# Performance work log

Measured on AMD Instinct MI355X. Metric: run time of the kernel, lower is better.

The kernel has to match this reference:

```python
import jax, jax.numpy as jnp
import numpy as np

B, S, D = 2, 2048, 2048
H, HD = 16, 128
ROPE_THETA = 10000.0


def _rope_cos_sin(seq_len, head_dim, dtype=jnp.float32):
    inv_freq = 1.0 / (ROPE_THETA ** (jnp.arange(0, head_dim, 2, dtype=jnp.float32) / head_dim))
    t = jnp.arange(seq_len, dtype=jnp.float32)
    freqs = jnp.outer(t, inv_freq)                     # [S, HD/2]
    emb = jnp.concatenate([freqs, freqs], axis=-1)     # [S, HD]
    return jnp.cos(emb).astype(dtype), jnp.sin(emb).astype(dtype)


def _rotate_half(x):
    x1, x2 = jnp.split(x, 2, axis=-1)
    return jnp.concatenate([-x2, x1], axis=-1)


def _apply_rope(x, cos, sin):
    # x: [B, S, H, HD]; cos/sin: [S, HD] -> broadcast over batch and heads
    c = cos[None, :, None, :]
    s = sin[None, :, None, :]
    return x * c + _rotate_half(x) * s


def setup_inputs() -> dict:
    key = jax.random.key(0)
    ks = jax.random.split(key, 6)
    scale = 1.0 / np.sqrt(D)
    hidden_states = jax.random.normal(ks[0], (B, S, D), dtype=jnp.float32)
    # causal additive mask: 0 on/below diagonal, large negative above
    neg = jnp.finfo(jnp.float32).min
    causal = jnp.where(jnp.tril(jnp.ones((S, S), dtype=bool)), 0.0, neg)
    attention_mask = jnp.broadcast_to(causal[None, None, :, :], (B, 1, S, S)).astype(jnp.float32)
    Wq = jax.random.normal(ks[1], (D, D), dtype=jnp.float32) * scale
    Wk = jax.random.normal(ks[2], (D, D), dtype=jnp.float32) * scale
    Wv = jax.random.normal(ks[3], (D, D), dtype=jnp.float32) * scale
    Wo = jax.random.normal(ks[4], (D, D), dtype=jnp.float32) * scale
    return {"hidden_states": hidden_states, "attention_mask": attention_mask,
            "Wq": Wq, "Wk": Wk, "Wv": Wv, "Wo": Wo}


def reference(hidden_states, attention_mask, Wq, Wk, Wv, Wo):
    b, s, d = hidden_states.shape
    # projections (torch Linear: x @ W^T)
    q = (hidden_states @ Wq.T).reshape(b, s, H, HD)
    k = (hidden_states @ Wk.T).reshape(b, s, H, HD)
    v = (hidden_states @ Wv.T).reshape(b, s, H, HD)
    cos, sin = _rope_cos_sin(s, HD, hidden_states.dtype)
    q = _apply_rope(q, cos, sin)
    k = _apply_rope(k, cos, sin)
    # naive attention, [B, H, S, S] scores materialized as in the original
    scores = jnp.einsum('bqhd,bkhd->bhqk', q, k) / np.sqrt(HD)
    scores = scores + attention_mask
    attn = jax.nn.softmax(scores, axis=-1)
    out = jnp.einsum('bhqk,bkhd->bqhd', attn, v).reshape(b, s, d)
    return out @ Wo.T
```

## Files before the change

kernel.cpp:

```cpp
#include <hip/hip_runtime.h>
#include <hip/hip_bf16.h>

typedef __hip_bfloat16 bf16;
typedef __attribute__((ext_vector_type(8))) short s16x8;
typedef __attribute__((ext_vector_type(4))) float f32x4;
typedef __attribute__((ext_vector_type(16))) float f32x16;

#define MFMA16(a, b, c) __builtin_amdgcn_mfma_f32_16x16x32_bf16(a, b, c, 0, 0, 0)
#define MFMA32(a, b, c) __builtin_amdgcn_mfma_f32_32x32x16_bf16(a, b, c, 0, 0, 0)

#define GLL16(gsrc, ldst)                                                                 \
  __builtin_amdgcn_global_load_lds(                                                       \
      (const __attribute__((address_space(1))) unsigned int*)(gsrc),                      \
      (__attribute__((address_space(3))) unsigned int*)(ldst), 16, 0, 0)

#define VMCNT(n) asm volatile("s_waitcnt vmcnt(" #n ")" ::: "memory")
#define BARRIER() __builtin_amdgcn_s_barrier()

static constexpr int S_LEN = 2048;
static constexpr int D_DIM = 2048;
static constexpr int NY = 6144;

union BF4 { ushort4 u; bf16 b[4]; };

__device__ inline unsigned pack2(float a, float b) {
  union { bf16 h[2]; unsigned u; } x;
  x.h[0] = __float2bfloat16(a);
  x.h[1] = __float2bfloat16(b);
  return x.u;
}

__global__ void convert_all(const float* __restrict__ X, const float* __restrict__ Wq,
                            const float* __restrict__ Wk, const float* __restrict__ Wv,
                            const float* __restrict__ Wo, bf16* __restrict__ Xb,
                            bf16* __restrict__ Wb, bf16* __restrict__ Wob,
                            float* __restrict__ cosT, float* __restrict__ sinT) {
  int gid = blockIdx.x * 256 + threadIdx.x;
  if (gid < 6291456) {
    int i4 = gid * 4;
    const float* src;
    bf16* dst;
    int off;
    if (i4 < 8388608) {
      src = X; dst = Xb; off = i4;
    } else {
      int j = i4 - 8388608;
      int seg = j >> 22;
      off = j & 4194303;
      if (seg == 0) { src = Wq; dst = Wb; }
      else if (seg == 1) { src = Wk; dst = Wb + 4194304; }
      else if (seg == 2) { src = Wv; dst = Wb + 8388608; }
      else { src = Wo; dst = Wob; }
    }
    float4 v = *(const float4*)(src + off);
    BF4 o;
    o.b[0] = __float2bfloat16(v.x);
    o.b[1] = __float2bfloat16(v.y);
    o.b[2] = __float2bfloat16(v.z);
    o.b[3] = __float2bfloat16(v.w);
    *(ushort4*)(dst + off) = o.u;
  } else {
    int t4 = (gid - 6291456) * 4;
    if (t4 < 131072) {
#pragma unroll
      for (int k = 0; k < 4; ++k) {
        int i = t4 + k;
        int d = i & 63, s = i >> 6;
        float inv = powf(10000.0f, -(float)d * (1.0f / 64.0f));
        float ang = (float)s * inv;
        cosT[i] = cosf(ang);
        sinT[i] = sinf(ang);
      }
    }
  }
}

__global__ __launch_bounds__(256) void rope_tv(bf16* __restrict__ Y,
                                               const float* __restrict__ cosT,
                                               const float* __restrict__ sinT,
                                               bf16* __restrict__ Vt) {
  __shared__ bf16 tile[32][36];
  const int bid = blockIdx.x;
  const int t = threadIdx.x;
  if (bid < 8192) {
    int idx = bid * 256 + t;
    int quad = idx & 15;
    int h = (idx >> 4) & 15;
    int m = (idx >> 8) & 4095;
    int g = idx >> 20;
    int s = m & (S_LEN - 1);
    int d0 = quad * 4;
    float sc = g ? 1.0f : 0.08838834764831845f * 1.4426950408889634f;
    bf16* p = Y + (size_t)m * NY + g * D_DIM + h * 128 + d0;
    BF4 lo, hi, olo, ohi;
    lo.u = *(const ushort4*)p;
    hi.u = *(const ushort4*)(p + 64);
    float4 c = *(const float4*)(cosT + s * 64 + d0);
    float4 sn = *(const float4*)(sinT + s * 64 + d0);
    float cc[4] = {c.x, c.y, c.z, c.w};
    float ss[4] = {sn.x, sn.y, sn.z, sn.w};
#pragma unroll
    for (int i = 0; i < 4; ++i) {
      float x1 = __bfloat162float(lo.b[i]);
      float x2 = __bfloat162float(hi.b[i]);
      olo.b[i] = __float2bfloat16((x1 * cc[i] - x2 * ss[i]) * sc);
      ohi.b[i] = __float2bfloat16((x2 * cc[i] + x1 * ss[i]) * sc);
    }
    *(ushort4*)p = olo.u;
    *(ushort4*)(p + 64) = ohi.u;
  } else {
    int id = bid - 8192;
    int bx = id & 63, by = (id >> 6) & 3, bh = id >> 8;
    int b = bh >> 4, h = bh & 15;
    int s0 = bx * 32, d0 = by * 32;
    int r = t >> 3;
    int c4 = (t & 7) * 4;
    BF4 in;
    in.u = *(const ushort4*)(Y + (size_t)(b * S_LEN + s0 + r) * NY + 4096 + h * 128 + d0 + c4);
    *(ushort4*)(&tile[r][c4]) = in.u;
    __syncthreads();
    BF4 o;
#pragma unroll
    for (int i = 0; i < 4; ++i) o.b[i] = tile[c4 + i][r];
    *(ushort4*)(Vt + (size_t)bh * 128 * S_LEN + (size_t)(d0 + r) * S_LEN + s0 + c4) = o.u;
  }
}

__device__ inline void storeC(float* p, float v) { *p = v; }
__device__ inline void storeC(bf16* p, float v) { *p = __float2bfloat16(v); }

__global__ __launch_bounds__(512, 2) void gemm256(const bf16* __restrict__ A,
                                                  const bf16* __restrict__ Bm,
                                                  bf16* __restrict__ C, int K, int lda,
                                                  int ldb, int ldc, int mt) {
  __shared__ __align__(16) char lds[131072];
  char* A0buf = lds;
  char* B0buf = lds + 32768;
  char* A1buf = lds + 65536;
  char* B1buf = lds + 98304;
  const int tid = threadIdx.x;
  const int lane = tid & 63;
  const int w = tid >> 6;
  const int wm = w >> 2, wn = w & 3;
  const int l15 = lane & 15, lh4 = lane >> 4;
  const int xr = l15 & 7;
  const int xo0 = ((lh4 ^ xr) << 4);
  const int xo1 = (((4 + lh4) ^ xr) << 4);

  const int nwg = gridDim.x;
  const int bid = blockIdx.x;
  const int swz = (bid & 7) * (nwg >> 3) + (bid >> 3);
  const int bm = swz % mt, bn = swz / mt;
  const int row0 = bm * 256, col0 = bn * 256;

  const int srow8 = lane >> 3;
  const int scol = ((lane & 7) ^ srow8) * 8;
  const bf16* gA_s = A + (size_t)(row0 + w * 8 + srow8) * lda + scol;
  const bf16* gB_s = Bm + (size_t)(col0 + (w >> 2) * 64 + (w & 3) * 8 + srow8) * ldb + scol;
  const int ldst = w * 1024;

#define STAGE_A(bufa, rh, k0)                                                     \
  {                                                                               \
    GLL16(gA_s + (size_t)((rh)*64) * lda + (k0), (bufa) + (rh)*16384 + ldst);     \
    GLL16(gA_s + (size_t)((rh)*64 + 128) * lda + (k0),                            \
          (bufa) + (rh)*16384 + 8192 + ldst);                                     \
  }
#define STAGE_B(bufb, ch, k0)                                                     \
  {                                                                               \
    GLL16(gB_s + (size_t)((ch)*32) * ldb + (k0), (bufb) + (ch)*16384 + ldst);     \
    GLL16(gB_s + (size_t)((ch)*32 + 128) * ldb + (k0),                            \
          (bufb) + (ch)*16384 + 8192 + ldst);                                     \
  }

  f32x4 acc[8][4];
#pragma unroll
  for (int i = 0; i < 8; ++i)
#pragma unroll
    for (int j = 0; j < 4; ++j) acc[i][j] = (f32x4){0.f, 0.f, 0.f, 0.f};

  s16x8 af[4][2];
  s16x8 bfr[2][2];

#define READ_AH(bufa, rh)                                                         \
  _Pragma("unroll") for (int ii = 0; ii < 4; ++ii) {                              \
    const char* p_ = (bufa) + (rh)*16384 + (wm * 64 + ii * 16 + l15) * 128;       \
    af[ii][0] = *(const s16x8*)(p_ + xo0);                                        \
    af[ii][1] = *(const s16x8*)(p_ + xo1);                                        \
  }
#define READ_BH(bufb, ch)                                                         \
  _Pragma("unroll") for (int jj = 0; jj < 2; ++jj) {                              \
    const char* p_ = (bufb) + (ch)*16384 + (wn * 32 + jj * 16 + l15) * 128;       \
    bfr[jj][0] = *(const s16x8*)(p_ + xo0);                                       \
    bfr[jj][1] = *(const s16x8*)(p_ + xo1);                                       \
  }
#define QUAD(rh, ch)                                                              \
  __builtin_amdgcn_s_setprio(1);                                                  \
  _Pragma("unroll") for (int jj = 0; jj < 2; ++jj)                                \
  _Pragma("unroll") for (int ii = 0; ii < 4; ++ii)                                \
  _Pragma("unroll") for (int ks = 0; ks < 2; ++ks)                                \
      acc[(rh)*4 + ii][(ch)*2 + jj] =                                             \
          MFMA16(af[ii][ks], bfr[jj][ks], acc[(rh)*4 + ii][(ch)*2 + jj]);         \
  __builtin_amdgcn_s_setprio(0);

  STAGE_A(A0buf, 0, 0);
  STAGE_B(B0buf, 0, 0);
  STAGE_B(B0buf, 1, 0);
  STAGE_A(A0buf, 1, 0);
  STAGE_A(A1buf, 0, 64);
  STAGE_B(B1buf, 1, 64);
  STAGE_A(A1buf, 1, 64);
  VMCNT(6);
  BARRIER();

  const int NI = K >> 7;
  for (int i = 0; i < NI; ++i) {
    const int kT1 = (2 * i + 1) << 6;
    const int kT2 = (2 * i + 2) << 6;
    const int kT3 = (2 * i + 3) << 6;
    const bool nl = (i + 1 < NI);
    READ_AH(A0buf, 0);
    READ_BH(B0buf, 0);
    STAGE_B(B1buf, 0, kT1);
    BARRIER();
    QUAD(0, 0);
    BARRIER();
    READ_BH(B0buf, 1);
    if (nl) STAGE_A(A0buf, 0, kT2);
    BARRIER();
    QUAD(0, 1);
    BARRIER();
    READ_AH(A0buf, 1);
    if (nl) STAGE_B(B0buf, 1, kT2);
    BARRIER();
    QUAD(1, 1);
    BARRIER();
    READ_BH(B0buf, 0);
    if (nl) STAGE_A(A0buf, 1, kT2);
    BARRIER();
    QUAD(1, 0);
    if (nl) { VMCNT(6); } else { VMCNT(0); }
    BARRIER();
    READ_AH(A1buf, 0);
    READ_BH(B1buf, 0);
    if (nl) STAGE_B(B0buf, 0, kT2);
    BARRIER();
    QUAD(0, 0);
    BARRIER();
    READ_BH(B1buf, 1);
    if (nl) STAGE_A(A1buf, 0, kT3);
    BARRIER();
    QUAD(0, 1);
    BARRIER();
    READ_AH(A1buf, 1);
    if (nl) STAGE_B(B1buf, 1, kT3);
    BARRIER();
    QUAD(1, 1);
    BARRIER();
    READ_BH(B1buf, 0);
    if (nl) STAGE_A(A1buf, 1, kT3);
    BARRIER();
    QUAD(1, 0);
    if (nl) { VMCNT(6); }
    BARRIER();
  }
#undef STAGE_A
#undef STAGE_B
#undef READ_AH
#undef READ_BH
#undef QUAD

#pragma unroll
  for (int ri = 0; ri < 8; ++ri)
#pragma unroll
    for (int cj = 0; cj < 4; ++cj) {
      int gr = row0 + wm * 128 + ri * 16 + lh4 * 4;
      int gc = col0 + wn * 64 + cj * 16 + l15;
#pragma unroll
      for (int rr = 0; rr < 4; ++rr)
        C[(size_t)(gr + rr) * ldc + gc] = __float2bfloat16(acc[ri][cj][rr]);
    }
}

template <typename OutT>
__global__ __launch_bounds__(512, 2) void gemm_fine(const bf16* __restrict__ A,
                                                    const bf16* __restrict__ Bm,
                                                    OutT* __restrict__ C, int K, int lda,
                                                    int ldb, int ldc, int mt) {
  __shared__ __align__(16) char lds[147456];
  char* b0 = lds;
  char* b1 = lds + 49152;
  char* b2 = lds + 98304;
  const int tid = threadIdx.x;
  const int lane = tid & 63;
  const int w = tid >> 6;
  const int wm = w >> 2, wn = w & 3;
  const int l15 = lane & 15, lh4 = lane >> 4;
  const int xr = l15 & 7;
  const int xo0 = ((lh4 ^ xr) << 4);
  const int xo1 = (((4 + lh4) ^ xr) << 4);

  const int nwg = gridDim.x;
  const int bid = blockIdx.x;
  const int swz = (bid & 7) * (nwg >> 3) + (bid >> 3);
  const int bm = swz % mt, bn = swz / mt;
  const int row0 = bm * 128, col0 = bn * 256;

  const int srow = w * 8 + (lane >> 3);
  const int scol = ((lane & 7) ^ (lane >> 3)) * 8;
  const bf16* gA = A + (size_t)(row0 + srow) * lda + scol;
  const bf16* gB = Bm + (size_t)(col0 + srow) * ldb + scol;
  const int ldst = w * 1024;

  f32x4 acc[4][4];
#pragma unroll
  for (int i = 0; i < 4; ++i)
#pragma unroll
    for (int j = 0; j < 4; ++j) acc[i][j] = (f32x4){0.f, 0.f, 0.f, 0.f};

  s16x8 af[4], bfr[4];

#define PH_READ(BUF, XO)                                                          \
  _Pragma("unroll") for (int ii = 0; ii < 4; ++ii)                                \
      af[ii] = *(const s16x8*)((BUF) + (wm * 64 + ii * 16 + l15) * 128 + (XO));   \
  _Pragma("unroll") for (int jj = 0; jj < 4; ++jj)                                \
      bfr[jj] = *(const s16x8*)((BUF) + 16384 + (wn * 64 + jj * 16 + l15) * 128 + (XO));
#define PH_FMA()                                                                  \
  __builtin_amdgcn_s_setprio(1);                                                  \
  _Pragma("unroll") for (int jj = 0; jj < 4; ++jj)                                \
  _Pragma("unroll") for (int ii = 0; ii < 4; ++ii)                                \
      acc[ii][jj] = MFMA16(af[ii], bfr[jj], acc[ii][jj]);                         \
  __builtin_amdgcn_s_setprio(0);
#define STAGE_T(BUF, kS)                                                          \
  GLL16(gA + (kS), (BUF) + ldst);                                                 \
  GLL16(gA + (size_t)64 * lda + (kS), (BUF) + 8192 + ldst);                       \
  GLL16(gB + (kS), (BUF) + 16384 + ldst);                                         \
  GLL16(gB + (size_t)64 * ldb + (kS), (BUF) + 24576 + ldst);                      \
  GLL16(gB + (size_t)128 * ldb + (kS), (BUF) + 32768 + ldst);                     \
  GLL16(gB + (size_t)192 * ldb + (kS), (BUF) + 40960 + ldst);
#define TILE_MAIN(RBUF, SBUF, kS)                                                 \
  PH_READ(RBUF, xo0);                                                             \
  GLL16(gA + (kS), (SBUF) + ldst);                                                \
  GLL16(gA + (size_t)64 * lda + (kS), (SBUF) + 8192 + ldst);                      \
  GLL16(gB + (kS), (SBUF) + 16384 + ldst);                                        \
  BARRIER();                                                                      \
  PH_FMA();                                                                       \
  BARRIER();                                                                      \
  PH_READ(RBUF, xo1);                                                             \
  GLL16(gB + (size_t)64 * ldb + (kS), (SBUF) + 24576 + ldst);                     \
  GLL16(gB + (size_t)128 * ldb + (kS), (SBUF) + 32768 + ldst);                    \
  GLL16(gB + (size_t)192 * ldb + (kS), (SBUF) + 40960 + ldst);                    \
  BARRIER();                                                                      \
  PH_FMA();                                                                       \
  VMCNT(6);                                                                       \
  BARRIER();

  STAGE_T(b0, 0);
  STAGE_T(b1, 64);
  VMCNT(6);
  BARRIER();

  const int NT = K >> 6;
  for (int t = 0; t < NT - 2; t += 3) {
    TILE_MAIN(b0, b2, (size_t)(t + 2) * 64);
    TILE_MAIN(b1, b0, (size_t)(t + 3) * 64);
    TILE_MAIN(b2, b1, (size_t)(t + 4) * 64);
  }
  PH_READ(b0, xo0);
  BARRIER();
  PH_FMA();
  BARRIER();
  PH_READ(b0, xo1);
  BARRIER();
  PH_FMA();
  VMCNT(0);
  BARRIER();
  PH_READ(b1, xo0);
  BARRIER();
  PH_FMA();
  BARRIER();
  PH_READ(b1, xo1);
  BARRIER();
  PH_FMA();
#undef PH_READ
#undef PH_FMA
#undef STAGE_T
#undef TILE_MAIN

#pragma unroll
  for (int mi = 0; mi < 4; ++mi)
#pragma unroll
    for (int ni = 0; ni < 4; ++ni) {
      int gr = row0 + wm * 64 + mi * 16 + lh4 * 4;
      int gc = col0 + wn * 64 + ni * 16 + l15;
#pragma unroll
      for (int rr = 0; rr < 4; ++rr)
        storeC(&C[(size_t)(gr + rr) * ldc + gc], acc[mi][ni][rr]);
    }
}

__global__ __launch_bounds__(256, 2) void attn_fwd(const bf16* __restrict__ Y,
                                                   const bf16* __restrict__ Vt,
                                                   bf16* __restrict__ At) {
  __shared__ __align__(16) char smem[65536];

  const int idx = blockIdx.x;
  const int qt = (idx < 256) ? (15 - (idx >> 5)) : ((idx - 256) >> 5);
  const int bh = idx & 31;
  const int b = bh >> 4, h = bh & 15;
  const int tid = threadIdx.x;
  const int lane = tid & 63;
  const int w = tid >> 6;
  const int l31 = lane & 31;
  const int hi = lane >> 5;
  const int q0w = qt * 128 + w * 32;
  const int q = q0w + l31;

  s16x8 qf[8];
  {
    const bf16* qb = Y + (size_t)(b * S_LEN + q) * NY + h * 128 + hi * 8;
#pragma unroll
    for (int s = 0; s < 8; ++s) qf[s] = *(const s16x8*)(qb + s * 16);
  }

  f32x16 O[4];
#pragma unroll
  for (int d = 0; d < 4; ++d)
#pragma unroll
    for (int e = 0; e < 16; ++e) O[d][e] = 0.f;
  float m_run = -3.0e38f, l_run = 0.f;

  const bf16* Kbase = Y + (size_t)(b * S_LEN) * NY + 2048 + h * 128;
  const bf16* Vbase = Vt + (size_t)bh * 128 * S_LEN;
  const int tmax = 2 * qt + 1;

  const int rk_ = w * 4 + (lane >> 4);
  const int ck_ = lane & 15;
  const int dv_ = w * 8 + (lane >> 3);
  const int cv_ = lane & 7;

#define STAGE_KV(T, BASE)                                                         \
  {                                                                               \
    const int kv0s = (T)*64;                                                      \
    _Pragma("unroll") for (int j = 0; j < 4; ++j) {                               \
      int rk = j * 16 + rk_;                                                      \
      GLL16(Kbase + (size_t)(kv0s + rk) * NY + ((ck_ ^ (rk & 15)) * 8),           \
            (BASE) + (j * 4096 + w * 1024));                                      \
      int dv = j * 32 + dv_;                                                      \
      GLL16(Vbase + (size_t)dv * S_LEN + kv0s + ((cv_ ^ (dv & 7)) * 8),           \
            (BASE) + 16384 + (j * 4096 + w * 1024));                              \
    }                                                                             \
  }

  STAGE_KV(0, smem);

  for (int t = 0; t <= tmax; ++t) {
    const int kv0 = t * 64;
    const char* cur = smem + (t & 1) * 32768;
    BARRIER();
    if (t < tmax) {
      STAGE_KV(t + 1, smem + ((t + 1) & 1) * 32768);
      VMCNT(8);
    } else {
      VMCNT(0);
    }
    BARRIER();
    if (kv0 > q0w + 31) continue;

    float sv[32];
#pragma unroll
    for (int tt = 0; tt < 2; ++tt) {
      f32x16 sa;
#pragma unroll
      for (int e = 0; e < 16; ++e) sa[e] = 0.f;
      const int rk = tt * 32 + l31;
      const char* kr = cur + rk * 256;
      const int xr = (rk & 15) << 4;
      __builtin_amdgcn_s_setprio(1);
#pragma unroll
      for (int s = 0; s < 8; ++s) {
        s16x8 kf = *(const s16x8*)(kr + ((s * 32 + hi * 16) ^ xr));
        sa = MFMA32(kf, qf[s], sa);
      }
      __builtin_amdgcn_s_setprio(0);
#pragma unroll
      for (int e = 0; e < 16; ++e) sv[tt * 16 + e] = sa[e];
    }

    if (kv0 + 63 > q0w) {
#pragma unroll
      for (int tt = 0; tt < 2; ++tt)
#pragma unroll
        for (int r = 0; r < 16; ++r) {
          int kvr = kv0 + tt * 32 + (r & 3) + 8 * (r >> 2) + 4 * hi;
          if (kvr > q) sv[tt * 16 + r] = -3.0e38f;
        }
    }

    float m8[8];
#pragma unroll
    for (int i = 0; i < 8; ++i)
      m8[i] = fmaxf(fmaxf(sv[i], sv[i + 8]), fmaxf(sv[i + 16], sv[i + 24]));
    float m2a = fmaxf(fmaxf(m8[0], m8[1]), fmaxf(m8[2], m8[3]));
    float m2b = fmaxf(fmaxf(m8[4], m8[5]), fmaxf(m8[6], m8[7]));
    float pmax = fmaxf(fmaxf(m2a, m2b), __shfl_xor(fmaxf(m2a, m2b), 32, 64));

    bool need = pmax > m_run + 11.54f;
    if (__any(need)) {
      float newm = fmaxf(m_run, pmax);
      float ef = exp2f(m_run - newm);
      m_run = newm;
      l_run *= ef;
#pragma unroll
      for (int d = 0; d < 4; ++d)
#pragma unroll
        for (int e = 0; e < 16; ++e) O[d][e] *= ef;
    }

#pragma unroll
    for (int i = 0; i < 32; ++i) sv[i] = exp2f(sv[i] - m_run);
    float s16v[16];
#pragma unroll
    for (int i = 0; i < 16; ++i) s16v[i] = sv[i] + sv[i + 16];
    float s8v[8];
#pragma unroll
    for (int i = 0; i < 8; ++i) s8v[i] = s16v[i] + s16v[i + 8];
    float s4v[4];
#pragma unroll
    for (int i = 0; i < 4; ++i) s4v[i] = s8v[i] + s8v[i + 4];
    float rsum = (s4v[0] + s4v[1]) + (s4v[2] + s4v[3]);
    rsum += __shfl_xor(rsum, 32, 64);
    l_run += rsum;

    unsigned pw[4][4];
#pragma unroll
    for (int tt = 0; tt < 2; ++tt) {
      const int bs = tt * 16;
      unsigned x01 = pack2(sv[bs + 0], sv[bs + 1]);
      unsigned x23 = pack2(sv[bs + 2], sv[bs + 3]);
      unsigned x45 = pack2(sv[bs + 4], sv[bs + 5]);
      unsigned x67 = pack2(sv[bs + 6], sv[bs + 7]);
      unsigned y01 = pack2(sv[bs + 8], sv[bs + 9]);
      unsigned y23 = pack2(sv[bs + 10], sv[bs + 11]);
      unsigned y45 = pack2(sv[bs + 12], sv[bs + 13]);
      unsigned y67 = pack2(sv[bs + 14], sv[bs + 15]);
      asm volatile("v_permlane32_swap_b32 %0, %1" : "+v"(x01), "+v"(x45));
      asm volatile("v_permlane32_swap_b32 %0, %1" : "+v"(x23), "+v"(x67));
      asm volatile("v_permlane32_swap_b32 %0, %1" : "+v"(y01), "+v"(y45));
      asm volatile("v_permlane32_swap_b32 %0, %1" : "+v"(y23), "+v"(y67));
      pw[tt * 2][0] = x01;
      pw[tt * 2][1] = x23;
      pw[tt * 2][2] = x45;
      pw[tt * 2][3] = x67;
      pw[tt * 2 + 1][0] = y01;
      pw[tt * 2 + 1][1] = y23;
      pw[tt * 2 + 1][2] = y45;
      pw[tt * 2 + 1][3] = y67;
    }

#pragma unroll
    for (int dt = 0; dt < 4; ++dt) {
      const int d = dt * 32 + l31;
      const char* vr = cur + 16384 + d * 128;
      const int xv = (d & 7) << 4;
      __builtin_amdgcn_s_setprio(1);
#pragma unroll
      for (int sl = 0; sl < 4; ++sl) {
        s16x8 vf = *(const s16x8*)(vr + ((sl * 32 + hi * 16) ^ xv));
        union { unsigned u[4]; s16x8 v; } pb;
        pb.u[0] = pw[sl][0];
        pb.u[1] = pw[sl][1];
        pb.u[2] = pw[sl][2];
        pb.u[3] = pw[sl][3];
        O[dt] = MFMA32(vf, pb.v, O[dt]);
      }
      __builtin_amdgcn_s_setprio(0);
    }
  }
#undef STAGE_KV

  __syncthreads();
  const float inv = 1.0f / l_run;
  {
    const int orow = w * 32 + l31;
    const int xo = (orow & 15) << 4;
    char* obase = (char*)smem + orow * 256;
#pragma unroll
    for (int dt = 0; dt < 4; ++dt)
#pragma unroll
      for (int r = 0; r < 16; ++r) {
        int d = dt * 32 + (r & 3) + 8 * (r >> 2) + 4 * hi;
        *(bf16*)(obase + ((d * 2) ^ xo)) = __float2bfloat16(O[dt][r] * inv);
      }
  }
  __syncthreads();
  bf16* dst = At + (size_t)(b * S_LEN + qt * 128) * D_DIM + h * 128;
#pragma unroll
  for (int j = 0; j < 8; ++j) {
    int id = j * 256 + tid;
    int rr = id >> 4, cc = id & 15;
    int4 val = *(const int4*)((char*)smem + rr * 256 + ((cc * 16) ^ ((rr & 15) << 4)));
    *(int4*)(dst + (size_t)rr * D_DIM + cc * 8) = val;
  }
}

extern "C" void kernel_launch(void* const* d_in, const int* in_sizes, int n_in,
                              void* d_out, int out_size, void* d_ws, size_t ws_size,
                              hipStream_t stream) {
  const float* X = (const float*)d_in[0];
  const float* Wq = (const float*)d_in[2];
  const float* Wk = (const float*)d_in[3];
  const float* Wv = (const float*)d_in[4];
  const float* Wo = (const float*)d_in[5];
  float* out = (float*)d_out;
  char* ws = (char*)d_ws;

  bf16* Xb = (bf16*)(ws);
  bf16* Wb = (bf16*)(ws + 16777216);
  bf16* Wob = (bf16*)(ws + 41943040);
  bf16* Y = (bf16*)(ws + 50331648);
  bf16* Vt = (bf16*)(ws + 100663296);
  bf16* At = (bf16*)(ws + 117440512);
  float* cosT = (float*)(ws + 134217728);
  float* sinT = (float*)(ws + 134742016);

  convert_all<<<24704, 256, 0, stream>>>(X, Wq, Wk, Wv, Wo, Xb, Wb, Wob, cosT, sinT);

  gemm256<<<256, 512, 0, stream>>>(Xb, Wb, Y, 2048, 2048, 2048, 6144, 16);
  gemm_fine<bf16><<<256, 512, 0, stream>>>(Xb, Wb + (size_t)4096 * 2048, Y + 4096,
                                           2048, 2048, 2048, 6144, 32);
  rope_tv<<<16384, 256, 0, stream>>>(Y, cosT, sinT, Vt);
  attn_fwd<<<512, 256, 0, stream>>>(Y, Vt, At);
  gemm_fine<float><<<256, 512, 0, stream>>>(At, Wob, out, 2048, 2048, 2048, 2048, 32);
}
```

Before: 245.8 us.

## Fuse V transpose into V-projection GEMM epilogue and split QK MFMA accumulator chain

```diff
diff --git a/kernel.cpp b/kernel.cpp
--- a/kernel.cpp
+++ b/kernel.cpp
@@ -75,55 +75,34 @@
   }
 }
 
-__global__ __launch_bounds__(256) void rope_tv(bf16* __restrict__ Y,
+__global__ __launch_bounds__(256) void rope_qk(bf16* __restrict__ Y,
                                                const float* __restrict__ cosT,
-                                               const float* __restrict__ sinT,
-                                               bf16* __restrict__ Vt) {
-  __shared__ bf16 tile[32][36];
-  const int bid = blockIdx.x;
-  const int t = threadIdx.x;
-  if (bid < 8192) {
-    int idx = bid * 256 + t;
-    int quad = idx & 15;
-    int h = (idx >> 4) & 15;
-    int m = (idx >> 8) & 4095;
-    int g = idx >> 20;
-    int s = m & (S_LEN - 1);
-    int d0 = quad * 4;
-    float sc = g ? 1.0f : 0.08838834764831845f * 1.4426950408889634f;
-    bf16* p = Y + (size_t)m * NY + g * D_DIM + h * 128 + d0;
-    BF4 lo, hi, olo, ohi;
-    lo.u = *(const ushort4*)p;
-    hi.u = *(const ushort4*)(p + 64);
-    float4 c = *(const float4*)(cosT + s * 64 + d0);
-    float4 sn = *(const float4*)(sinT + s * 64 + d0);
-    float cc[4] = {c.x, c.y, c.z, c.w};
-    float ss[4] = {sn.x, sn.y, sn.z, sn.w};
-#pragma unroll
-    for (int i = 0; i < 4; ++i) {
-      float x1 = __bfloat162float(lo.b[i]);
-      float x2 = __bfloat162float(hi.b[i]);
-      olo.b[i] = __float2bfloat16((x1 * cc[i] - x2 * ss[i]) * sc);
-      ohi.b[i] = __float2bfloat16((x2 * cc[i] + x1 * ss[i]) * sc);
-    }
-    *(ushort4*)p = olo.u;
-    *(ushort4*)(p + 64) = ohi.u;
-  } else {
-    int id = bid - 8192;
-    int bx = id & 63, by = (id >> 6) & 3, bh = id >> 8;
-    int b = bh >> 4, h = bh & 15;
-    int s0 = bx * 32, d0 = by * 32;
-    int r = t >> 3;
-    int c4 = (t & 7) * 4;
-    BF4 in;
-    in.u = *(const ushort4*)(Y + (size_t)(b * S_LEN + s0 + r) * NY + 4096 + h * 128 + d0 + c4);
-    *(ushort4*)(&tile[r][c4]) = in.u;
-    __syncthreads();
-    BF4 o;
-#pragma unroll
-    for (int i = 0; i < 4; ++i) o.b[i] = tile[c4 + i][r];
-    *(ushort4*)(Vt + (size_t)bh * 128 * S_LEN + (size_t)(d0 + r) * S_LEN + s0 + c4) = o.u;
-  }
+                                               const float* __restrict__ sinT) {
+  int idx = blockIdx.x * 256 + threadIdx.x;
+  int quad = idx & 15;
+  int h = (idx >> 4) & 15;
+  int m = (idx >> 8) & 4095;
+  int g = idx >> 20;
+  int s = m & (S_LEN - 1);
+  int d0 = quad * 4;
+  float sc = g ? 1.0f : 0.08838834764831845f * 1.4426950408889634f;
+  bf16* p = Y + (size_t)m * NY + g * D_DIM + h * 128 + d0;
+  BF4 lo, hi, olo, ohi;
+  lo.u = *(const ushort4*)p;
+  hi.u = *(const ushort4*)(p + 64);
+  float4 c = *(const float4*)(cosT + s * 64 + d0);
+  float4 sn = *(const float4*)(sinT + s * 64 + d0);
+  float cc[4] = {c.x, c.y, c.z, c.w};
+  float ss[4] = {sn.x, sn.y, sn.z, sn.w};
+#pragma unroll
+  for (int i = 0; i < 4; ++i) {
+    float x1 = __bfloat162float(lo.b[i]);
+    float x2 = __bfloat162float(hi.b[i]);
+    olo.b[i] = __float2bfloat16((x1 * cc[i] - x2 * ss[i]) * sc);
+    ohi.b[i] = __float2bfloat16((x2 * cc[i] + x1 * ss[i]) * sc);
+  }
+  *(ushort4*)p = olo.u;
+  *(ushort4*)(p + 64) = ohi.u;
 }
 
 __device__ inline void storeC(float* p, float v) { *p = v; }
@@ -281,7 +260,7 @@
     }
 }
 
-template <typename OutT>
+template <typename OutT, bool TRANSV>
 __global__ __launch_bounds__(512, 2) void gemm_fine(const bf16* __restrict__ A,
                                                     const bf16* __restrict__ Bm,
                                                     OutT* __restrict__ C, int K, int lda,
@@ -386,16 +365,32 @@
 #undef STAGE_T
 #undef TILE_MAIN
 
-#pragma unroll
-  for (int mi = 0; mi < 4; ++mi)
-#pragma unroll
-    for (int ni = 0; ni < 4; ++ni) {
-      int gr = row0 + wm * 64 + mi * 16 + lh4 * 4;
-      int gc = col0 + wn * 64 + ni * 16 + l15;
-#pragma unroll
-      for (int rr = 0; rr < 4; ++rr)
-        storeC(&C[(size_t)(gr + rr) * ldc + gc], acc[mi][ni][rr]);
-    }
+  if constexpr (TRANSV) {
+    bf16* Vt = (bf16*)C;
+#pragma unroll
+    for (int mi = 0; mi < 4; ++mi)
+#pragma unroll
+      for (int ni = 0; ni < 4; ++ni) {
+        int gr = row0 + wm * 64 + mi * 16 + lh4 * 4;
+        int gc = col0 + wn * 64 + ni * 16 + l15;
+        size_t vrow = (size_t)((gr >> 11) * 2048 + gc);
+        BF4 o;
+#pragma unroll
+        for (int rr = 0; rr < 4; ++rr) o.b[rr] = __float2bfloat16(acc[mi][ni][rr]);
+        *(ushort4*)(Vt + vrow * S_LEN + (gr & (S_LEN - 1))) = o.u;
+      }
+  } else {
+#pragma unroll
+    for (int mi = 0; mi < 4; ++mi)
+#pragma unroll
+      for (int ni = 0; ni < 4; ++ni) {
+        int gr = row0 + wm * 64 + mi * 16 + lh4 * 4;
+        int gc = col0 + wn * 64 + ni * 16 + l15;
+#pragma unroll
+        for (int rr = 0; rr < 4; ++rr)
+          storeC(&C[(size_t)(gr + rr) * ldc + gc], acc[mi][ni][rr]);
+      }
+  }
 }
 
 __global__ __launch_bounds__(256, 2) void attn_fwd(const bf16* __restrict__ Y,
@@ -469,21 +464,23 @@
     float sv[32];
 #pragma unroll
     for (int tt = 0; tt < 2; ++tt) {
-      f32x16 sa;
-#pragma unroll
-      for (int e = 0; e < 16; ++e) sa[e] = 0.f;
+      f32x16 se, so;
+#pragma unroll
+      for (int e = 0; e < 16; ++e) { se[e] = 0.f; so[e] = 0.f; }
       const int rk = tt * 32 + l31;
       const char* kr = cur + rk * 256;
       const int xr = (rk & 15) << 4;
       __builtin_amdgcn_s_setprio(1);
 #pragma unroll
-      for (int s = 0; s < 8; ++s) {
-        s16x8 kf = *(const s16x8*)(kr + ((s * 32 + hi * 16) ^ xr));
-        sa = MFMA32(kf, qf[s], sa);
+      for (int s = 0; s < 8; s += 2) {
+        s16x8 kf0 = *(const s16x8*)(kr + ((s * 32 + hi * 16) ^ xr));
+        se = MFMA32(kf0, qf[s], se);
+        s16x8 kf1 = *(const s16x8*)(kr + (((s + 1) * 32 + hi * 16) ^ xr));
+        so = MFMA32(kf1, qf[s + 1], so);
       }
       __builtin_amdgcn_s_setprio(0);
 #pragma unroll
-      for (int e = 0; e < 16; ++e) sv[tt * 16 + e] = sa[e];
+      for (int e = 0; e < 16; ++e) sv[tt * 16 + e] = se[e] + so[e];
     }
 
     if (kv0 + 63 > q0w) {
@@ -626,9 +623,9 @@
   convert_all<<<24704, 256, 0, stream>>>(X, Wq, Wk, Wv, Wo, Xb, Wb, Wob, cosT, sinT);
 
   gemm256<<<256, 512, 0, stream>>>(Xb, Wb, Y, 2048, 2048, 2048, 6144, 16);
-  gemm_fine<bf16><<<256, 512, 0, stream>>>(Xb, Wb + (size_t)4096 * 2048, Y + 4096,
-                                           2048, 2048, 2048, 6144, 32);
-  rope_tv<<<16384, 256, 0, stream>>>(Y, cosT, sinT, Vt);
+  gemm_fine<bf16, true><<<256, 512, 0, stream>>>(Xb, Wb + (size_t)4096 * 2048, Vt,
+                                                 2048, 2048, 2048, 2048, 32);
+  rope_qk<<<8192, 256, 0, stream>>>(Y, cosT, sinT);
   attn_fwd<<<512, 256, 0, stream>>>(Y, Vt, At);
-  gemm_fine<float><<<256, 512, 0, stream>>>(At, Wob, out, 2048, 2048, 2048, 2048, 32);
+  gemm_fine<float, false><<<256, 512, 0, stream>>>(At, Wob, out, 2048, 2048, 2048, 2048, 32);
 }
```

After: 244.2 us. No clear change (-0.7%).
